# Kernel optimization log

Hardware: AMD Instinct MI355X
Metric: run time of the kernel (lower is better)

Reference implementation:

```python
import jax, jax.numpy as jnp
import numpy as np

IN_DIM = 500
BATCH = 131072
NBSECTOR = 11
NBMQ = 10
X_THRESHOLD = 0.001
INF_SCALE = 100.0
ZSTAR = 1000.0
CARD_UPPER = 70.0
CARD_LOWER = 69.0


def setup_inputs() -> dict:
    key = jax.random.key(0)
    ks = jax.random.split(key, 7)
    x = jax.random.uniform(ks[0], (BATCH, IN_DIM), dtype=jnp.float32)
    x_bw = jax.random.uniform(ks[1], (IN_DIM,), dtype=jnp.float32)
    alpha = jax.random.normal(ks[2], (IN_DIM,), dtype=jnp.float32)
    beta = jax.random.normal(ks[3], (IN_DIM,), dtype=jnp.float32)
    # risk matrix: small-magnitude so the quadratic form dQd is in a sane range
    Omega = 0.001 * jax.random.normal(ks[4], (IN_DIM, IN_DIM), dtype=jnp.float32)
    sector_id = jax.random.randint(ks[5], (IN_DIM,), 0, NBSECTOR, dtype=jnp.int32)
    mq_id = jax.random.randint(ks[6], (IN_DIM,), 0, NBMQ, dtype=jnp.int32)
    return {"x": x, "x_bw": x_bw, "alpha": alpha, "beta": beta,
            "Omega": Omega, "sector_id": sector_id, "mq_id": mq_id}


def reference(x, x_bw, alpha, beta, Omega, sector_id, mq_id):
    relu = jax.nn.relu
    d = x - x_bw                      # [B, D]
    abs_d = jnp.abs(d)
    sx = jnp.sum(x, axis=1)           # [B]

    tot = relu(1.0 - sx) + relu(sx - 1.0)
    tot = tot + relu(jnp.sum(abs_d, axis=1) - 0.05)

    # per-group masked sums (replaces the one-hot matvec loops):
    # segment-sum over the feature axis, then |.|, relu, sum over groups.
    sec = jax.ops.segment_sum(d.T, sector_id, num_segments=NBSECTOR).T  # [B, NBSECTOR]
    tot = tot + jnp.sum(relu(jnp.abs(sec) - 0.1), axis=1)
    mqs = jax.ops.segment_sum(d.T, mq_id, num_segments=NBMQ).T          # [B, NBMQ]
    tot = tot + jnp.sum(relu(jnp.abs(mqs) - 0.1), axis=1)

    tot = tot + relu(jnp.abs(d @ beta) - 0.1)

    # eval-mode cardinality constraint (train=False branch): hard count
    nnz = jnp.sum((x > X_THRESHOLD).astype(x.dtype), axis=1)
    tot = tot + relu(nnz - CARD_UPPER) + relu(CARD_LOWER - nnz)

    # NOTE: original sums |d| over the WHOLE batch (scalar), faithfully kept
    l_all = 0.5 * jnp.sum(abs_d)
    tot = tot + relu(0.6 - l_all)

    dQd = jnp.sum((d @ Omega) * d, axis=1)  # quadratic form per row
    tot = tot + relu(dQd - 0.01) + relu(0.0025 - dQd)

    l2 = d @ alpha
    # MONTH == 0 branch of the original
    tot = tot + relu(100.0 * dQd - 100.0 * l2 - ZSTAR)

    fea_probs = relu(1.0 - jnp.tanh(tot / INF_SCALE))
    return fea_probs
```

## Files before the change

### kernel.cpp

```cpp
#include <hip/hip_runtime.h>
#include <hip/hip_bf16.h>

#define D_IN  500
#define BATCH 131072
#define BM    64

typedef unsigned short u16;
typedef unsigned int   u32;
using f32x4  = __attribute__((ext_vector_type(4))) float;
using bf16x8 = __attribute__((ext_vector_type(8))) short;

__device__ __forceinline__ u16 f2bf(float f) {
  u32 b = __builtin_bit_cast(u32, f);
  b += 0x7FFFu + ((b >> 16) & 1u);
  return (u16)(b >> 16);
}
__device__ __forceinline__ float bf2f(u32 hbits) {
  return __builtin_bit_cast(float, hbits << 16);
}

__device__ __forceinline__ float xla_tanh(float z) {
  float xc = fminf(fmaxf(z, -7.90531110764903f), 7.90531110764903f);
  float x2 = xc * xc;
  float p = fmaf(x2, -2.76076847742355e-16f, 2.00018790482477e-13f);
  p = fmaf(x2, p, -8.60467152213735e-11f);
  p = fmaf(x2, p,  5.12229709037114e-08f);
  p = fmaf(x2, p,  1.48572235717979e-05f);
  p = fmaf(x2, p,  6.37261928875436e-04f);
  p = fmaf(x2, p,  4.89352455891786e-03f);
  p = xc * p;
  float q = fmaf(x2, 1.19825839466702e-06f, 1.18534705686654e-04f);
  q = fmaf(x2, q, 2.26843463243900e-03f);
  q = fmaf(x2, q, 4.89352518554385e-03f);
  return (fabsf(z) < 0.0004f) ? z : (p / q);
}

__global__ void disc_prep(const float* __restrict__ Omega,
                          const float* __restrict__ alpha,
                          const float* __restrict__ beta,
                          const int* __restrict__ sector_id,
                          const int* __restrict__ mq_id,
                          u16* __restrict__ wsA,
                          float* __restrict__ l_all) {
  int idx = blockIdx.x * 256 + threadIdx.x;
  if (idx == 0) *l_all = 0.0f;
  if (idx >= 544 * 512) return;
  int blk    = idx >> 9;
  int within = idx & 511;
  int lane   = within >> 3;
  int e      = within & 7;
  int n, j;
  if (blk < 512) {
    int chunk = blk >> 5;
    int nw    = (blk >> 4) & 1;
    int jg    = (blk >> 2) & 3;
    int ks    = blk & 3;
    n = chunk * 32 + nw * 16 + (lane & 15);
    j = jg * 128 + ks * 32 + ((lane >> 4) << 3) + e;
  } else {
    int b4  = blk - 512;
    int sub = b4 >> 2;
    int ks  = b4 & 3;
    int nw = sub >> 2, jg = sub & 3;
    n = 512 + nw * 16 + (lane & 15);
    j = jg * 128 + ks * 32 + ((lane >> 4) << 3) + e;
  }
  float v = 0.0f;
  if (j < D_IN) {
    if (n < D_IN)       v = Omega[j * D_IN + n];
    else if (n < 512)   v = 0.0f;
    else if (n < 523)   v = (sector_id[j] == (n - 512)) ? 1.0f : 0.0f;
    else if (n < 533)   v = (mq_id[j]     == (n - 523)) ? 1.0f : 0.0f;
    else if (n == 533)  v = beta[j];
    else if (n == 534)  v = alpha[j];
    else if (n == 535)  v = 1.0f;
  }
  wsA[idx] = f2bf(v);
}

__global__ __launch_bounds__(512, 2) void disc_main(
    const float* __restrict__ x, const float* __restrict__ x_bw,
    const u16* __restrict__ wsA,
    float* __restrict__ tot_out, float* __restrict__ l_all) {
  __shared__ alignas(16) u16 ldsA[BM * 512];
  __shared__ float s_ext[BM][25];
  __shared__ float s_dqd[BM][8];
  __shared__ float s_sabs[BM];
  __shared__ float s_nnz[BM];
  __shared__ float s_sxbw;

  const int t = threadIdx.x;
  const float* xblk = x + (size_t)blockIdx.x * (BM * D_IN);

  for (int z = t; z < BM * 25; z += 512) ((float*)s_ext)[z] = 0.0f;

  for (int z = t; z < BM * 12; z += 512) {
    int r = z / 12, c = 500 + (z - r * 12);
    int byte = ((r << 10) + (c << 1)) ^ ((r & 7) << 4);
    *(u16*)((char*)ldsA + byte) = 0;
  }

  for (int v4 = t; v4 < (BM * D_IN) / 4; v4 += 512) {
    int f = v4 << 2;
    int r = f / D_IN;
    int c = f - r * D_IN;
    float4 xv = *(const float4*)(xblk + f);
    float4 bw = *(const float4*)(x_bw + c);
    u32 lo = (u32)f2bf(xv.x - bw.x) | ((u32)f2bf(xv.y - bw.y) << 16);
    u32 hi = (u32)f2bf(xv.z - bw.z) | ((u32)f2bf(xv.w - bw.w) << 16);
    int byte = ((r << 10) + (c << 1)) ^ ((r & 7) << 4);
    *(uint2*)((char*)ldsA + byte) = make_uint2(lo, hi);
  }

  {
    int r = t >> 3, s = t & 7;
    const float* xr = xblk + r * D_IN;
    float sabs = 0.f, nnz = 0.f, sxbw = 0.f;
    for (int c = s; c < D_IN; c += 8) {
      float xv = xr[c], bw = x_bw[c];
      sabs += fabsf(xv - bw);
      nnz  += (xv > 0.001f) ? 1.0f : 0.0f;
      sxbw += bw;
    }
    #pragma unroll
    for (int m = 1; m < 8; m <<= 1) {
      sabs += __shfl_xor(sabs, m, 64);
      nnz  += __shfl_xor(nnz,  m, 64);
      sxbw += __shfl_xor(sxbw, m, 64);
    }
    if (s == 0) { s_sabs[r] = sabs; s_nnz[r] = nnz; }
    if (t == 0) s_sxbw = sxbw;
  }

  __syncthreads();

  const int l   = t & 63;
  const int w   = t >> 6;
  const int nw  = w >> 2;
  const int jg  = w & 3;
  const int l15 = l & 15;
  const int l4  = l >> 4;
  const f32x4 fzero = {0.f, 0.f, 0.f, 0.f};

  bf16x8 bfs[4][4];
  #pragma unroll
  for (int ks = 0; ks < 4; ++ks) {
    const int kk = jg * 128 + ks * 32 + l4 * 8;
    #pragma unroll
    for (int cf = 0; cf < 4; ++cf) {
      int i = cf * 16 + l15;
      int byte = ((i << 10) + (kk << 1)) ^ ((i & 7) << 4);
      bfs[ks][cf] = *(const bf16x8*)((const char*)ldsA + byte);
    }
  }

  float pdqd[4] = {0.f, 0.f, 0.f, 0.f};
  const u16* wA = wsA + (((nw * 16 + jg * 4) << 9)) + (l << 3);

  #pragma unroll 1
  for (int chunk = 0; chunk < 16; ++chunk) {
    bf16x8 af[4];
    #pragma unroll
    for (int ks = 0; ks < 4; ++ks)
      af[ks] = *(const bf16x8*)(wA + (((chunk * 32 + ks) << 9)));
    f32x4 acc[4] = {fzero, fzero, fzero, fzero};
    #pragma unroll
    for (int ks = 0; ks < 4; ++ks)
      #pragma unroll
      for (int cf = 0; cf < 4; ++cf)
        acc[cf] = __builtin_amdgcn_mfma_f32_16x16x32_bf16(af[ks], bfs[ks][cf], acc[cf], 0, 0, 0);
    const int nbase = chunk * 32 + nw * 16 + l4 * 4;
    #pragma unroll
    for (int cf = 0; cf < 4; ++cf) {
      int i = cf * 16 + l15;
      int byte = ((i << 10) + (nbase << 1)) ^ ((i & 7) << 4);
      uint2 dv = *(const uint2*)((const char*)ldsA + byte);
      pdqd[cf] += acc[cf][0] * bf2f(dv.x & 0xFFFFu)
                + acc[cf][1] * bf2f(dv.x >> 16)
                + acc[cf][2] * bf2f(dv.y & 0xFFFFu)
                + acc[cf][3] * bf2f(dv.y >> 16);
    }
  }

  {
    const int sub = nw * 4 + jg;
    f32x4 acc4[4];
    #pragma unroll
    for (int cf = 0; cf < 4; ++cf) acc4[cf] = fzero;
    #pragma unroll
    for (int ks = 0; ks < 4; ++ks) {
      bf16x8 afrag = *(const bf16x8*)(wsA + ((512 + sub * 4 + ks) << 9) + (l << 3));
      #pragma unroll
      for (int cf = 0; cf < 4; ++cf)
        acc4[cf] = __builtin_amdgcn_mfma_f32_16x16x32_bf16(afrag, bfs[ks][cf], acc4[cf], 0, 0, 0);
    }
    #pragma unroll
    for (int cf = 0; cf < 4; ++cf) {
      int i = cf * 16 + l15;
      #pragma unroll
      for (int q = 0; q < 4; ++q) {
        int n = 512 + nw * 16 + l4 * 4 + q;
        if (n < 536) atomicAdd(&s_ext[i][n - 512], acc4[cf][q]);
      }
    }
  }

  #pragma unroll
  for (int cf = 0; cf < 4; ++cf) {
    float v = pdqd[cf];
    v += __shfl_xor(v, 16, 64);
    v += __shfl_xor(v, 32, 64);
    if (l < 16) s_dqd[cf * 16 + l][w] = v;
  }
  __syncthreads();

  if (t < BM) {
    float dqd = 0.f;
    #pragma unroll
    for (int ww = 0; ww < 8; ++ww) dqd += s_dqd[t][ww];
    float tex = 0.f;
    #pragma unroll
    for (int c = 0; c < 22; ++c)
      tex += fmaxf(fabsf(s_ext[t][c]) - 0.1f, 0.f);
    float l2 = s_ext[t][22];
    float sx = s_ext[t][23] + s_sxbw;
    float sabs = s_sabs[t], nnz = s_nnz[t];
    float tot = tex
      + fmaxf(1.f - sx, 0.f) + fmaxf(sx - 1.f, 0.f)
      + fmaxf(sabs - 0.05f, 0.f)
      + fmaxf(nnz - 70.f, 0.f) + fmaxf(69.f - nnz, 0.f)
      + fmaxf(dqd - 0.01f, 0.f) + fmaxf(0.0025f - dqd, 0.f)
      + fmaxf(100.f * dqd - 100.f * l2 - 1000.f, 0.f);
    tot_out[(size_t)blockIdx.x * BM + t] = tot;
    float bs = sabs;
    #pragma unroll
    for (int m = 1; m < 64; m <<= 1) bs += __shfl_xor(bs, m, 64);
    if (t == 0) atomicAdd(l_all, bs);
  }
}

__global__ void disc_final(const float* __restrict__ tot_in,
                           const float* __restrict__ l_all,
                           float* __restrict__ out) {
  int i = blockIdx.x * 256 + threadIdx.x;
  if (i >= BATCH) return;
  float lterm = fmaxf(0.6f - 0.5f * (*l_all), 0.0f);
  float z = (tot_in[i] + lterm) * 0.01f;
  out[i] = fmaxf(1.0f - xla_tanh(z), 0.0f);
}

extern "C" void kernel_launch(void* const* d_in, const int* in_sizes, int n_in,
                              void* d_out, int out_size, void* d_ws, size_t ws_size,
                              hipStream_t stream) {
  const float* x     = (const float*)d_in[0];
  const float* x_bw  = (const float*)d_in[1];
  const float* alpha = (const float*)d_in[2];
  const float* beta  = (const float*)d_in[3];
  const float* Omega = (const float*)d_in[4];
  const int* sector_id = (const int*)d_in[5];
  const int* mq_id     = (const int*)d_in[6];
  float* out = (float*)d_out;

  char* ws = (char*)d_ws;
  u16*   wsA   = (u16*)ws;
  float* l_all = (float*)(ws + 544 * 1024);
  float* tot   = (float*)(ws + 544 * 1024 + 1024);

  disc_prep<<<1088, 256, 0, stream>>>(Omega, alpha, beta, sector_id, mq_id, wsA, l_all);
  disc_main<<<BATCH / BM, 512, 0, stream>>>(x, x_bw, wsA, tot, l_all);
  disc_final<<<BATCH / 256, 256, 0, stream>>>(tot, l_all, out);
}
```

Measured before the change: 541.1 us.

## Derive row abs-sum and nnz from LDS bf16 tiles, prefetch weight fragments

The second pass that re-read every x row from global memory to get the per-row |d| sum and nonzero count is removed. Those statistics are now computed from the bf16 d values already held in registers, compared against a precomputed threshold (0.001 - x_bw), and accumulated with LDS atomics. The x_bw sum is computed once in the prep kernel, the x-to-LDS load loop is unrolled with a multiply-shift division, and the weight fragments for the next chunk are prefetched before the current chunk's epilogue. The risk is that bf16 rounding of d changes the abs-sum and threshold comparisons slightly, and that the added atomics and prefetch registers raise register pressure.

After: 567.2 us. 1.05x slower.

```diff
diff --git a/kernel.cpp b/kernel.cpp
--- a/kernel.cpp
+++ b/kernel.cpp
@@ -38,12 +38,22 @@
 __global__ void disc_prep(const float* __restrict__ Omega,
                           const float* __restrict__ alpha,
                           const float* __restrict__ beta,
+                          const float* __restrict__ x_bw,
                           const int* __restrict__ sector_id,
                           const int* __restrict__ mq_id,
                           u16* __restrict__ wsA,
-                          float* __restrict__ l_all) {
+                          float* __restrict__ thr,
+                          float* __restrict__ smalls) {
   int idx = blockIdx.x * 256 + threadIdx.x;
-  if (idx == 0) *l_all = 0.0f;
+  if (idx == 1) smalls[1] = 0.0f;
+  if (idx < 512) thr[idx] = (idx < D_IN) ? (0.001f - x_bw[idx]) : 3.0e38f;
+  if (blockIdx.x == 0 && threadIdx.x < 64) {
+    float s = 0.f;
+    for (int c = threadIdx.x; c < D_IN; c += 64) s += x_bw[c];
+    #pragma unroll
+    for (int m = 1; m < 64; m <<= 1) s += __shfl_xor(s, m, 64);
+    if (threadIdx.x == 0) smalls[0] = s;
+  }
   if (idx >= 544 * 512) return;
   int blk    = idx >> 9;
   int within = idx & 511;
@@ -80,19 +90,20 @@
 
 __global__ __launch_bounds__(512, 2) void disc_main(
     const float* __restrict__ x, const float* __restrict__ x_bw,
-    const u16* __restrict__ wsA,
+    const u16* __restrict__ wsA, const float* __restrict__ thr,
+    const float* __restrict__ smalls,
     float* __restrict__ tot_out, float* __restrict__ l_all) {
   __shared__ alignas(16) u16 ldsA[BM * 512];
   __shared__ float s_ext[BM][25];
   __shared__ float s_dqd[BM][8];
   __shared__ float s_sabs[BM];
   __shared__ float s_nnz[BM];
-  __shared__ float s_sxbw;
 
   const int t = threadIdx.x;
   const float* xblk = x + (size_t)blockIdx.x * (BM * D_IN);
 
   for (int z = t; z < BM * 25; z += 512) ((float*)s_ext)[z] = 0.0f;
+  if (t < BM) { s_sabs[t] = 0.0f; s_nnz[t] = 0.0f; }
 
   for (int z = t; z < BM * 12; z += 512) {
     int r = z / 12, c = 500 + (z - r * 12);
@@ -100,36 +111,19 @@
     *(u16*)((char*)ldsA + byte) = 0;
   }
 
-  for (int v4 = t; v4 < (BM * D_IN) / 4; v4 += 512) {
-    int f = v4 << 2;
-    int r = f / D_IN;
-    int c = f - r * D_IN;
-    float4 xv = *(const float4*)(xblk + f);
-    float4 bw = *(const float4*)(x_bw + c);
-    u32 lo = (u32)f2bf(xv.x - bw.x) | ((u32)f2bf(xv.y - bw.y) << 16);
-    u32 hi = (u32)f2bf(xv.z - bw.z) | ((u32)f2bf(xv.w - bw.w) << 16);
-    int byte = ((r << 10) + (c << 1)) ^ ((r & 7) << 4);
-    *(uint2*)((char*)ldsA + byte) = make_uint2(lo, hi);
-  }
-
-  {
-    int r = t >> 3, s = t & 7;
-    const float* xr = xblk + r * D_IN;
-    float sabs = 0.f, nnz = 0.f, sxbw = 0.f;
-    for (int c = s; c < D_IN; c += 8) {
-      float xv = xr[c], bw = x_bw[c];
-      sabs += fabsf(xv - bw);
-      nnz  += (xv > 0.001f) ? 1.0f : 0.0f;
-      sxbw += bw;
-    }
-    #pragma unroll
-    for (int m = 1; m < 8; m <<= 1) {
-      sabs += __shfl_xor(sabs, m, 64);
-      nnz  += __shfl_xor(nnz,  m, 64);
-      sxbw += __shfl_xor(sxbw, m, 64);
-    }
-    if (s == 0) { s_sabs[r] = sabs; s_nnz[r] = nnz; }
-    if (t == 0) s_sxbw = sxbw;
+  #pragma unroll
+  for (int k = 0; k < 16; ++k) {
+    int v4 = t + k * 512;
+    if (v4 < (BM * D_IN) / 4) {
+      int r = (int)(((unsigned)v4 * 33555u) >> 22);
+      int c = v4 - r * 125;
+      float4 xv = *(const float4*)(xblk + r * D_IN + c * 4);
+      float4 bw = *(const float4*)(x_bw + c * 4);
+      u32 lo = (u32)f2bf(xv.x - bw.x) | ((u32)f2bf(xv.y - bw.y) << 16);
+      u32 hi = (u32)f2bf(xv.z - bw.z) | ((u32)f2bf(xv.w - bw.w) << 16);
+      int byte = ((r << 10) + (c << 3)) ^ ((r & 7) << 4);
+      *(uint2*)((char*)ldsA + byte) = make_uint2(lo, hi);
+    }
   }
 
   __syncthreads();
@@ -154,21 +148,56 @@
     }
   }
 
+  {
+    float psab[4] = {0.f, 0.f, 0.f, 0.f};
+    float pnnz[4] = {0.f, 0.f, 0.f, 0.f};
+    #pragma unroll
+    for (int kq = 0; kq < 2; ++kq) {
+      const int ks = nw * 2 + kq;
+      const int kk = jg * 128 + ks * 32 + l4 * 8;
+      float4 th0 = *(const float4*)(thr + kk);
+      float4 th1 = *(const float4*)(thr + kk + 4);
+      #pragma unroll
+      for (int cf = 0; cf < 4; ++cf) {
+        bf16x8 bv = bfs[ks][cf];
+        #pragma unroll
+        for (int e = 0; e < 8; ++e) {
+          float dv = bf2f((u32)(u16)bv[e]);
+          float th = (e < 4) ? ((const float*)&th0)[e] : ((const float*)&th1)[e - 4];
+          psab[cf] += fabsf(dv);
+          pnnz[cf] += (dv > th) ? 1.0f : 0.0f;
+        }
+      }
+    }
+    #pragma unroll
+    for (int cf = 0; cf < 4; ++cf) {
+      atomicAdd(&s_sabs[cf * 16 + l15], psab[cf]);
+      atomicAdd(&s_nnz[cf * 16 + l15], pnnz[cf]);
+    }
+  }
+
   float pdqd[4] = {0.f, 0.f, 0.f, 0.f};
-  const u16* wA = wsA + (((nw * 16 + jg * 4) << 9)) + (l << 3);
+  const u16* wAl = wsA + (l << 3);
+  const int fb0 = nw * 16 + jg * 4;
+
+  bf16x8 af[4];
+  #pragma unroll
+  for (int ks = 0; ks < 4; ++ks)
+    af[ks] = *(const bf16x8*)(wAl + ((fb0 + ks) << 9));
 
   #pragma unroll 1
   for (int chunk = 0; chunk < 16; ++chunk) {
-    bf16x8 af[4];
-    #pragma unroll
-    for (int ks = 0; ks < 4; ++ks)
-      af[ks] = *(const bf16x8*)(wA + (((chunk * 32 + ks) << 9)));
     f32x4 acc[4] = {fzero, fzero, fzero, fzero};
     #pragma unroll
     for (int ks = 0; ks < 4; ++ks)
       #pragma unroll
       for (int cf = 0; cf < 4; ++cf)
         acc[cf] = __builtin_amdgcn_mfma_f32_16x16x32_bf16(af[ks], bfs[ks][cf], acc[cf], 0, 0, 0);
+    const int nb = (chunk < 15) ? ((chunk + 1) * 32 + fb0)
+                                : (512 + (nw * 4 + jg) * 4);
+    #pragma unroll
+    for (int ks = 0; ks < 4; ++ks)
+      af[ks] = *(const bf16x8*)(wAl + ((nb + ks) << 9));
     const int nbase = chunk * 32 + nw * 16 + l4 * 4;
     #pragma unroll
     for (int cf = 0; cf < 4; ++cf) {
@@ -183,17 +212,14 @@
   }
 
   {
-    const int sub = nw * 4 + jg;
     f32x4 acc4[4];
     #pragma unroll
     for (int cf = 0; cf < 4; ++cf) acc4[cf] = fzero;
     #pragma unroll
-    for (int ks = 0; ks < 4; ++ks) {
-      bf16x8 afrag = *(const bf16x8*)(wsA + ((512 + sub * 4 + ks) << 9) + (l << 3));
+    for (int ks = 0; ks < 4; ++ks)
       #pragma unroll
       for (int cf = 0; cf < 4; ++cf)
-        acc4[cf] = __builtin_amdgcn_mfma_f32_16x16x32_bf16(afrag, bfs[ks][cf], acc4[cf], 0, 0, 0);
-    }
+        acc4[cf] = __builtin_amdgcn_mfma_f32_16x16x32_bf16(af[ks], bfs[ks][cf], acc4[cf], 0, 0, 0);
     #pragma unroll
     for (int cf = 0; cf < 4; ++cf) {
       int i = cf * 16 + l15;
@@ -223,7 +249,7 @@
     for (int c = 0; c < 22; ++c)
       tex += fmaxf(fabsf(s_ext[t][c]) - 0.1f, 0.f);
     float l2 = s_ext[t][22];
-    float sx = s_ext[t][23] + s_sxbw;
+    float sx = s_ext[t][23] + smalls[0];
     float sabs = s_sabs[t], nnz = s_nnz[t];
     float tot = tex
       + fmaxf(1.f - sx, 0.f) + fmaxf(sx - 1.f, 0.f)
@@ -262,11 +288,14 @@
   float* out = (float*)d_out;
 
   char* ws = (char*)d_ws;
-  u16*   wsA   = (u16*)ws;
-  float* l_all = (float*)(ws + 544 * 1024);
-  float* tot   = (float*)(ws + 544 * 1024 + 1024);
-
-  disc_prep<<<1088, 256, 0, stream>>>(Omega, alpha, beta, sector_id, mq_id, wsA, l_all);
-  disc_main<<<BATCH / BM, 512, 0, stream>>>(x, x_bw, wsA, tot, l_all);
-  disc_final<<<BATCH / 256, 256, 0, stream>>>(tot, l_all, out);
-}
+  u16*   wsA    = (u16*)ws;
+  float* thr    = (float*)(ws + 544 * 1024);
+  float* smalls = (float*)(ws + 544 * 1024 + 2048);
+  float* tot    = (float*)(ws + 544 * 1024 + 4096);
+
+  disc_prep<<<1088, 256, 0, stream>>>(Omega, alpha, beta, x_bw, sector_id, mq_id,
+                                      wsA, thr, smalls);
+  disc_main<<<BATCH / BM, 512, 0, stream>>>(x, x_bw, wsA, thr, smalls,
+                                            tot, smalls + 1);
+  disc_final<<<BATCH / 256, 256, 0, stream>>>(tot, smalls + 1, out);
+}
```
